# Kernel tuning notes

Measured on AMD Instinct MI355X. Metric: run time of the kernel, lower is better.

The kernel has to match this reference:

```python
import jax, jax.numpy as jnp
import numpy as np

B, N, C = 4, 2304, 256
H = 8                      # num_heads
D = C // H                 # head_dim = 32
SCALE = D ** -0.5
H_DS, W_DS = 48, 48
UP = 2                     # spatial_down_ratio
EPS = 1e-5


def setup_inputs() -> dict:
    key = jax.random.key(0)
    ks = jax.random.split(key, 16)
    g = lambda k, shape, s: (jax.random.normal(k, shape, dtype=jnp.float32) * s)
    return {
        "x1": g(ks[0], (B, N, C), 1.0),
        "x2": g(ks[1], (B, N, C), 1.0),
        # attention projections (torch Linear convention: [out, in], no bias)
        "q1_w": g(ks[2], (C, C), C ** -0.5),
        "kv1_w": g(ks[3], (2 * C, C), C ** -0.5),
        "q2_w": g(ks[4], (C, C), C ** -0.5),
        "kv2_w": g(ks[5], (2 * C, C), C ** -0.5),
        # per-head scalar biases
        "beta12": jnp.full((H,), 0.2, dtype=jnp.float32),
        "beta21": jnp.full((H,), 0.1, dtype=jnp.float32),
        # output projections
        "p1_w": g(ks[6], (C, C), (2.0 / C) ** 0.5),
        "p1_b": g(ks[7], (C,), 1e-2),
        "p2_w": g(ks[8], (C, C), (2.0 / C) ** 0.5),
        "p2_b": g(ks[9], (C,), 1e-2),
        # LayerNorm affine params
        "g1": jnp.ones((C,), dtype=jnp.float32),
        "b1": jnp.zeros((C,), dtype=jnp.float32),
        "g2": jnp.ones((C,), dtype=jnp.float32),
        "b2": jnp.zeros((C,), dtype=jnp.float32),
    }


def _heads(x):
    # [B,N,C] -> [B,H,N,D]
    return x.reshape(B, N, H, D).transpose(0, 2, 1, 3)


def _merge(x):
    # [B,H,N,D] -> [B,N,C]
    return x.transpose(0, 2, 1, 3).reshape(B, N, C)


def _cross_attn(q, k, v, beta):
    # scores: [B,H,N,N] with per-head scalar bias
    s = jnp.einsum("bhqd,bhkd->bhqk", q, k) * SCALE + beta[None, :, None, None]
    a = jax.nn.softmax(s, axis=-1)
    return jnp.einsum("bhqk,bhkd->bhqd", a, v)


def _layernorm(x, g, b):
    mu = jnp.mean(x, axis=-1, keepdims=True)
    var = jnp.var(x, axis=-1, keepdims=True)
    return (x - mu) * jax.lax.rsqrt(var + EPS) * g + b


def _forward(x1, x2, q1_w, kv1_w, q2_w, kv2_w, beta12, beta21,
             p1_w, p1_b, p2_w, p2_b, g1, b1, g2, b2):
    q1 = _heads(x1 @ q1_w.T)
    kv1 = x1 @ kv1_w.T          # [B,N,2C]
    k1, v1 = _heads(kv1[..., :C]), _heads(kv1[..., C:])
    q2 = _heads(x2 @ q2_w.T)
    kv2 = x2 @ kv2_w.T
    k2, v2 = _heads(kv2[..., :C]), _heads(kv2[..., C:])

    o1 = _merge(_cross_attn(q1, k2, v2, beta12))   # x1 attends to x2
    o2 = _merge(_cross_attn(q2, k1, v1, beta21))   # x2 attends to x1

    y1 = _layernorm(jax.nn.relu(o1 @ p1_w.T + p1_b), g1, b1)
    y2 = _layernorm(jax.nn.relu(o2 @ p2_w.T + p2_b), g2, b2)

    # [B,N,C] -> [B,C,H_ds,W_ds]
    y1 = y1.transpose(0, 2, 1).reshape(B, C, H_DS, W_DS)
    y2 = y2.transpose(0, 2, 1).reshape(B, C, H_DS, W_DS)

    # bilinear upsample x2, align_corners=False (half-pixel == jax.image default)
    out_shape = (B, C, H_DS * UP, W_DS * UP)
    y1 = jax.image.resize(y1, out_shape, method="bilinear")
    y2 = jax.image.resize(y2, out_shape, method="bilinear")
    return y1, y2


def reference(x1, x2, q1_w, kv1_w, q2_w, kv2_w, beta12, beta21,
              p1_w, p1_b, p2_w, p2_b, g1, b1, g2, b2):
    return _forward(x1, x2, q1_w, kv1_w, q2_w, kv2_w, beta12, beta21,
                    p1_w, p1_b, p2_w, p2_b, g1, b1, g2, b2)
```

## Files before the change

kernel.cpp:

```cpp
#include <hip/hip_runtime.h>
#include <math.h>


typedef __attribute__((ext_vector_type(8))) short short8;
typedef __attribute__((ext_vector_type(4))) float f32x4;
typedef __attribute__((ext_vector_type(16))) float f32x16;
typedef __attribute__((ext_vector_type(2))) unsigned uint32x2;

#define MFMA16(a, b, c) __builtin_amdgcn_mfma_f32_16x16x32_bf16((a), (b), (c), 0, 0, 0)
#define MFMA32(a, b, c) __builtin_amdgcn_mfma_f32_32x32x16_bf16((a), (b), (c), 0, 0, 0)

__device__ __forceinline__ float bf2f(ushort u) {
    union { unsigned u; float f; } x; x.u = ((unsigned)u) << 16; return x.f;
}
__device__ __forceinline__ ushort f2bf(float f) {
    union { float f; unsigned u; } x; x.f = f;
    unsigned u = x.u;
    return (ushort)((u + 0x7fffu + ((u >> 16) & 1u)) >> 16);
}
__device__ __forceinline__ unsigned cvt_pk_bf16(float a, float b) {
    unsigned r;
    asm("v_cvt_pk_bf16_f32 %0, %1, %2" : "=v"(r) : "v"(a), "v"(b));
    return r;
}
__device__ __forceinline__ float fast_ex2(float x) {
    float r;
    asm("v_exp_f32 %0, %1" : "=v"(r) : "v"(x));
    return r;
}
__device__ __forceinline__ void plswap(unsigned &a, unsigned &b) {
    uint32x2 r = __builtin_amdgcn_permlane32_swap(a, b, false, false);
    a = r[0]; b = r[1];
}

__global__ void sniff_kernel(const ushort* __restrict__ x, int* __restrict__ flag)
{
    int lane = threadIdx.x;
    ushort u = x[lane * 2];
    int e = (u >> 7) & 0xFF;
    int outlier = (e < 100 || e > 135) ? 1 : 0;
    unsigned long long m = __ballot(outlier);
    if (lane == 0) *flag = (__popcll(m) >= 16) ? 1 : 0;
}

__global__ __launch_bounds__(256) void convert_params(
    const void* s0, const void* s1, const void* s2, const void* s3,
    const void* s4, const void* s5, const void* s6, const void* s7,
    const void* s8, const void* s9, const void* s10, const void* s11,
    ushort* __restrict__ dst, const int* __restrict__ flag)
{
    int idx = blockIdx.x * 256 + threadIdx.x;
    if (idx >= 525824) return;
    const void* src; int off;
    if      (idx < 65536)  { src = s0;  off = idx; }
    else if (idx < 196608) { src = s1;  off = idx - 65536; }
    else if (idx < 262144) { src = s2;  off = idx - 196608; }
    else if (idx < 393216) { src = s3;  off = idx - 262144; }
    else if (idx < 458752) { src = s4;  off = idx - 393216; }
    else if (idx < 524288) { src = s5;  off = idx - 458752; }
    else if (idx < 524544) { src = s6;  off = idx - 524288; }
    else if (idx < 524800) { src = s7;  off = idx - 524544; }
    else if (idx < 525056) { src = s8;  off = idx - 524800; }
    else if (idx < 525312) { src = s9;  off = idx - 525056; }
    else if (idx < 525568) { src = s10; off = idx - 525312; }
    else                   { src = s11; off = idx - 525568; }
    ushort v = (*flag) ? f2bf(((const float*)src)[off])
                       : ((const ushort*)src)[off];
    dst[idx] = v;
}

__global__ __launch_bounds__(256) void convert_x(
    const void* __restrict__ x1, const void* __restrict__ x2,
    ushort* __restrict__ o1, ushort* __restrict__ o2,
    const int* __restrict__ flag)
{
    int idx = blockIdx.x * 256 + threadIdx.x;
    int which = idx >= 294912;
    int off = (which ? idx - 294912 : idx) * 8;
    const void* src = which ? x2 : x1;
    ushort* dst = which ? o2 : o1;
    if (*flag) {
        const float* p = (const float*)src + off;
        float4 a = *(const float4*)p;
        float4 c = *(const float4*)(p + 4);
        uint4 u;
        u.x = cvt_pk_bf16(a.x, a.y);
        u.y = cvt_pk_bf16(a.z, a.w);
        u.z = cvt_pk_bf16(c.x, c.y);
        u.w = cvt_pk_bf16(c.z, c.w);
        *(uint4*)(dst + off) = u;
    } else {
        *(uint4*)(dst + off) = *(const uint4*)((const ushort*)src + off);
    }
}

__global__ __launch_bounds__(256) void gemm_bt(
    const void* __restrict__ Ain, const ushort* __restrict__ W,
    ushort* __restrict__ C, const ushort* __restrict__ bias,
    int M, int N, int K, int relu, const int* __restrict__ dflag, int a_ext,
    int mode, ushort* __restrict__ Kh, ushort* __restrict__ Vt,
    const ushort* __restrict__ W2, const ushort* __restrict__ bias2,
    ushort* __restrict__ Kh2, ushort* __restrict__ Vt2, int mhalf)
{
    __shared__ __align__(16) ushort As[64][40];
    __shared__ __align__(16) ushort Ws[64][40];

    const int m0 = blockIdx.x * 64;
    const int n0 = blockIdx.y * 64;
    const int tid = threadIdx.x;
    const int w = tid >> 6;
    const int lane = tid & 63;
    const int lm = lane & 15;
    const int quad = lane >> 4;
    const int a32 = a_ext ? *dflag : 0;

    const int side = (mhalf && m0 >= mhalf) ? 1 : 0;
    const ushort* Wu = side ? W2 : W;
    const ushort* bu = side ? bias2 : bias;
    ushort* Khu = side ? Kh2 : Kh;
    ushort* Vtu = side ? Vt2 : Vt;

    const f32x4 Z4 = {0.f, 0.f, 0.f, 0.f};
    f32x4 acc[4];
    for (int j = 0; j < 4; j++) acc[j] = Z4;

    const ushort* A16 = (const ushort*)Ain;
    const float*  A32 = (const float*)Ain;
    const int row = tid >> 2, off = (tid & 3) * 8;

    for (int k0 = 0; k0 < K; k0 += 32) {
        __syncthreads();
        if (a32) {
            const float* p0 = A32 + (size_t)(m0 + row) * K + k0 + off;
            float4 f0 = *(const float4*)p0;
            float4 f1 = *(const float4*)(p0 + 4);
            uint4 t0;
            t0.x = cvt_pk_bf16(f0.x, f0.y);
            t0.y = cvt_pk_bf16(f0.z, f0.w);
            t0.z = cvt_pk_bf16(f1.x, f1.y);
            t0.w = cvt_pk_bf16(f1.z, f1.w);
            *(uint4*)&As[row][off] = t0;
        } else {
            *(uint4*)&As[row][off] =
                *(const uint4*)(A16 + (size_t)(m0 + row) * K + k0 + off);
        }
        *(uint4*)&Ws[row][off] =
            *(const uint4*)(Wu + (size_t)(n0 + row) * K + k0 + off);
        __syncthreads();

        short8 af = *(const short8*)&As[w * 16 + lm][quad * 8];
        for (int nt = 0; nt < 4; nt++) {
            short8 wf = *(const short8*)&Ws[nt * 16 + lm][quad * 8];
            acc[nt] = MFMA16(af, wf, acc[nt]);
        }
    }

    const int grow = m0 + w * 16 + quad * 4;
    const int grel = grow - (side ? mhalf : 0);
    if (mode == 1) {
        const float QSC = 0.17677669529663687f * 1.4426950408889634f;
        int bb = grel / 2304;
        int tok = grel - bb * 2304;
        for (int nt = 0; nt < 4; nt++) {
            int col = n0 + nt * 16 + lm;
            if (col < 256) {
                for (int r = 0; r < 4; r++)
                    C[(size_t)(grow + r) * 256 + col] = f2bf(acc[nt][r] * QSC);
            } else if (col < 512) {
                int c2 = col - 256, hh = c2 >> 5, d = c2 & 31;
                for (int r = 0; r < 4; r++)
                    Khu[(((size_t)bb * 8 + hh) * 2304 + tok + r) * 32 + d] = f2bf(acc[nt][r]);
            } else {
                int c2 = col - 512, hh = c2 >> 5, d = c2 & 31;
                uint2 o;
                o.x = cvt_pk_bf16(acc[nt][0], acc[nt][1]);
                o.y = cvt_pk_bf16(acc[nt][2], acc[nt][3]);
                *(uint2*)&Vtu[(((size_t)bb * 8 + hh) * 32 + d) * 2304 + tok] = o;
            }
        }
    } else {
        for (int nt = 0; nt < 4; nt++) {
            int col = n0 + nt * 16 + lm;
            float bv = bu ? bf2f(bu[col]) : 0.f;
            for (int r = 0; r < 4; r++) {
                float v = acc[nt][r] + bv;
                if (relu) v = fmaxf(v, 0.f);
                C[(size_t)(grow + r) * N + col] = f2bf(v);
            }
        }
    }
}

__global__ __launch_bounds__(128) void attn_kernel(
    const ushort* __restrict__ Qa, const ushort* __restrict__ Kha,
    const ushort* __restrict__ Vta, ushort* __restrict__ Oa,
    const ushort* __restrict__ Qb, const ushort* __restrict__ Khb2,
    const ushort* __restrict__ Vtb2, ushort* __restrict__ Ob)
{
    const int sid = blockIdx.x;
    const int qb = blockIdx.y;
    const int side = sid >> 5;
    const int bh = sid & 31;
    const ushort* Q  = side ? Qb   : Qa;
    const ushort* Kh = side ? Khb2 : Kha;
    const ushort* Vt = side ? Vtb2 : Vta;
    ushort* O        = side ? Ob   : Oa;

    const int b = bh >> 3, h = bh & 7;
    const int tid = threadIdx.x;
    const int w = tid >> 6, lane = tid & 63;
    const int l31 = lane & 31, hl = lane >> 5;

    const int qrow = qb * 64 + w * 32 + l31;
    const ushort* qp = Q + ((size_t)b * 2304 + qrow) * 256 + h * 32 + hl * 8;
    const short8 qf0 = *(const short8*)qp;
    const short8 qf1 = *(const short8*)(qp + 16);

    f32x16 o0, o1;
    #pragma unroll
    for (int i = 0; i < 16; i++) { o0[i] = 0.f; o1[i] = 0.f; }
    const f32x16 Z16 = o0;
    float l = 0.f;

    const ushort* kp0 = Kh + (size_t)bh * 2304 * 32 + (size_t)l31 * 32 + hl * 8;
    const ushort* vp0 = Vt + (size_t)bh * 32 * 2304 + (size_t)l31 * 2304 + hl * 8;

#define LOADT(kf0v, kf1v, vf0v, vf1v, t) { \
    const ushort* _kp = kp0 + (size_t)(t) * 1024; \
    kf0v = *(const short8*)_kp; \
    kf1v = *(const short8*)(_kp + 16); \
    const ushort* _vp = vp0 + (t) * 32; \
    vf0v = *(const short8*)_vp; \
    vf1v = *(const short8*)(_vp + 16); \
}
#define COMP(kf0v, kf1v, vf0v, vf1v, oacc) { \
    f32x16 s = MFMA32(kf0v, qf0, Z16); \
    s = MFMA32(kf1v, qf1, s); \
    float p[16]; \
    _Pragma("unroll") \
    for (int i = 0; i < 16; i++) p[i] = fast_ex2(s[i]); \
    l += (((p[0] + p[1]) + (p[2] + p[3])) + ((p[4] + p[5]) + (p[6] + p[7]))) \
       + (((p[8] + p[9]) + (p[10] + p[11])) + ((p[12] + p[13]) + (p[14] + p[15]))); \
    unsigned c0 = cvt_pk_bf16(p[0],  p[1]); \
    unsigned c1 = cvt_pk_bf16(p[2],  p[3]); \
    unsigned c2 = cvt_pk_bf16(p[4],  p[5]); \
    unsigned c3 = cvt_pk_bf16(p[6],  p[7]); \
    unsigned c4 = cvt_pk_bf16(p[8],  p[9]); \
    unsigned c5 = cvt_pk_bf16(p[10], p[11]); \
    unsigned c6 = cvt_pk_bf16(p[12], p[13]); \
    unsigned c7 = cvt_pk_bf16(p[14], p[15]); \
    plswap(c0, c2); plswap(c1, c3); plswap(c4, c6); plswap(c5, c7); \
    union { unsigned u[4]; short8 s8; } pA, pB; \
    pA.u[0] = c0; pA.u[1] = c1; pA.u[2] = c2; pA.u[3] = c3; \
    pB.u[0] = c4; pB.u[1] = c5; pB.u[2] = c6; pB.u[3] = c7; \
    oacc = MFMA32(vf0v, pA.s8, oacc); \
    oacc = MFMA32(vf1v, pB.s8, oacc); \
}

    short8 ka0, ka1, va0, va1;
    short8 kb0, kb1, vb0, vb1;

    LOADT(ka0, ka1, va0, va1, 0);
    LOADT(kb0, kb1, vb0, vb1, 1);

    for (int t = 0; t < 72; t += 2) {
        COMP(ka0, ka1, va0, va1, o0);
        { int ta = t + 2 < 72 ? t + 2 : 70; LOADT(ka0, ka1, va0, va1, ta); }
        COMP(kb0, kb1, vb0, vb1, o1);
        { int tb = t + 3 < 72 ? t + 3 : 71; LOADT(kb0, kb1, vb0, vb1, tb); }
    }
#undef LOADT
#undef COMP

    l += __shfl_xor(l, 32, 64);
    float rl = 1.f / l;
    ushort* op = O + ((size_t)b * 2304 + qrow) * 256 + h * 32 + hl * 4;
    #pragma unroll
    for (int g = 0; g < 4; g++) {
        float e0 = (o0[4 * g]     + o1[4 * g])     * rl;
        float e1 = (o0[4 * g + 1] + o1[4 * g + 1]) * rl;
        float e2 = (o0[4 * g + 2] + o1[4 * g + 2]) * rl;
        float e3 = (o0[4 * g + 3] + o1[4 * g + 3]) * rl;
        uint2 o;
        o.x = cvt_pk_bf16(e0, e1);
        o.y = cvt_pk_bf16(e2, e3);
        *(uint2*)(op + 8 * g) = o;
    }
}

__global__ __launch_bounds__(256) void lnt_kernel(
    const ushort* __restrict__ Z, const ushort* __restrict__ G1,
    const ushort* __restrict__ B1, const ushort* __restrict__ G2,
    const ushort* __restrict__ B2, ushort* __restrict__ Yt)
{
    __shared__ ushort T[256][72];

    const int tid = threadIdx.x;
    const int tok0 = blockIdx.x * 32;
    const int half = (tok0 >= 9216) ? 1 : 0;
    const int tr = tok0 - half * 9216;
    const int bb = tr / 2304;
    const int tokb = tr - bb * 2304;

    const int tok_l = tid >> 3;
    const int cq = tid & 7;

    const ushort* zp = Z + ((size_t)(tok0 + tok_l)) * 256 + cq * 32;
    uint dd[16];
    for (int i = 0; i < 4; i++) {
        uint4 v = *(const uint4*)(zp + i * 8);
        dd[i * 4 + 0] = v.x; dd[i * 4 + 1] = v.y;
        dd[i * 4 + 2] = v.z; dd[i * 4 + 3] = v.w;
    }
    float s = 0.f, q = 0.f;
    for (int e = 0; e < 16; e++) {
        float x0 = bf2f((ushort)dd[e]);
        float x1 = bf2f((ushort)(dd[e] >> 16));
        s += x0 + x1;
        q += x0 * x0 + x1 * x1;
    }
    s += __shfl_xor(s, 1, 64); q += __shfl_xor(q, 1, 64);
    s += __shfl_xor(s, 2, 64); q += __shfl_xor(q, 2, 64);
    s += __shfl_xor(s, 4, 64); q += __shfl_xor(q, 4, 64);
    float mu = s * (1.f / 256.f);
    float var = q * (1.f / 256.f) - mu * mu;
    float rs = rsqrtf(var + 1e-5f);

    const ushort* Gs = half ? G2 : G1;
    const ushort* Bs = half ? B2 : B1;
    const int col = tok_l + 4 * cq;

    for (int i = 0; i < 4; i++) {
        int cb = cq * 32 + i * 8;
        uint4 gv = *(const uint4*)(Gs + cb);
        uint4 bv = *(const uint4*)(Bs + cb);
        uint gg[4] = {gv.x, gv.y, gv.z, gv.w};
        uint bw[4] = {bv.x, bv.y, bv.z, bv.w};
        for (int k = 0; k < 4; k++) {
            uint u = dd[i * 4 + k];
            float x0 = bf2f((ushort)u), x1 = bf2f((ushort)(u >> 16));
            float y0 = (x0 - mu) * rs * bf2f((ushort)gg[k]) + bf2f((ushort)bw[k]);
            float y1 = (x1 - mu) * rs * bf2f((ushort)(gg[k] >> 16))
                     + bf2f((ushort)(bw[k] >> 16));
            int c = cb + 2 * k;
            T[c][col]     = f2bf(y0);
            T[c + 1][col] = f2bf(y1);
        }
    }
    __syncthreads();

    const int c_row = tid >> 3;
    const int tq = (tid & 7) * 4;
    const size_t obase = ((size_t)((half * 4 + bb) * 256)) * 2304 + tokb + tq;
    for (int i = 0; i < 8; i++) {
        int c = c_row + 32 * i;
        uint2 v = *(const uint2*)&T[c][tq + 4 * i];
        *(uint2*)(Yt + obase + (size_t)c * 2304) = v;
    }
}

__global__ __launch_bounds__(256) void upsample_kernel(
    const ushort* __restrict__ Yt, float* __restrict__ out)
{
    int idx = blockIdx.x * 256 + threadIdx.x;
    int m  = idx % 48;
    int t  = idx / 48;
    int oi = t % 96;
    int bc = t / 96;

    float fi = oi * 0.5f - 0.25f;
    int i0 = (int)floorf(fi);
    float wi = fi - (float)i0;
    int i1 = i0 + 1 < 47 ? i0 + 1 : 47;
    i0 = i0 > 0 ? i0 : 0;
    int jm = m - 1 > 0 ? m - 1 : 0;
    int jp = m + 1 < 47 ? m + 1 : 47;

    const ushort* r0 = Yt + (size_t)bc * 2304 + i0 * 48;
    const ushort* r1 = Yt + (size_t)bc * 2304 + i1 * 48;
    float a0 = bf2f(r0[jm]), b0 = bf2f(r0[m]), c0 = bf2f(r0[jp]);
    float a1 = bf2f(r1[jm]), b1 = bf2f(r1[m]), c1 = bf2f(r1[jp]);
    float u = 1.f - wi;
    float ha = u * a0 + wi * a1;
    float hb = u * b0 + wi * b1;
    float hc = u * c0 + wi * c1;
    float2 o;
    o.x = 0.25f * ha + 0.75f * hb;
    o.y = 0.75f * hb + 0.25f * hc;
    *(float2*)(out + (size_t)bc * 9216 + oi * 96 + m * 2) = o;
}

extern "C" void kernel_launch(void* const* d_in, const int* in_sizes, int n_in,
                              void* d_out, int out_size, void* d_ws, size_t ws_size,
                              hipStream_t stream)
{
    (void)in_sizes; (void)n_in; (void)out_size; (void)ws_size;

    ushort* ws  = (ushort*)d_ws;
    ushort* Q1  = ws;
    ushort* Q2  = Q1  + 2359296;
    ushort* KV1 = Q2  + 2359296;
    ushort* KV2 = KV1 + 4718592;
    ushort* wc  = KV2 + 4718592;
    int*    dflag = (int*)(wc + 525824);

    ushort* cqkv1w = wc;
    ushort* cqkv2w = wc + 196608;
    ushort* cp1w  = wc + 393216;
    ushort* cp2w  = wc + 458752;
    ushort* cp1b  = wc + 524288;
    ushort* cp2b  = wc + 524544;
    ushort* cg1   = wc + 524800;
    ushort* cb1   = wc + 525056;
    ushort* cg2   = wc + 525312;
    ushort* cb2   = wc + 525568;

    float*  outf = (float*)d_out;
    ushort* O1  = (ushort*)d_out;
    ushort* O2  = O1 + 2359296;
    ushort* Xb1 = O2 + 2359296;
    ushort* Xb2 = Xb1 + 2359296;
    ushort* Z1  = KV2;
    ushort* Yt  = Q1;
    (void)Q2; (void)O2; (void)Xb2;

    dim3 blk(256);
    sniff_kernel<<<dim3(1), dim3(64), 0, stream>>>((const ushort*)d_in[0], dflag);
    convert_params<<<dim3(2054), blk, 0, stream>>>(
        d_in[2], d_in[3], d_in[4], d_in[5], d_in[8], d_in[10],
        d_in[9], d_in[11], d_in[12], d_in[13], d_in[14], d_in[15],
        wc, dflag);
    convert_x<<<dim3(2304), blk, 0, stream>>>(d_in[0], d_in[1], Xb1, Xb2, dflag);

    gemm_bt<<<dim3(288, 12), blk, 0, stream>>>(Xb1, cqkv1w, Q1, nullptr,
        18432, 768, 256, 0, dflag, 0, 1, KV1, KV1 + 2359296,
        cqkv2w, nullptr, KV2, KV2 + 2359296, 9216);

    attn_kernel<<<dim3(64, 36), dim3(128), 0, stream>>>(
        Q1, KV2, KV2 + 2359296, O1,
        Q2, KV1, KV1 + 2359296, O2);

    gemm_bt<<<dim3(288, 4), blk, 0, stream>>>(O1, cp1w, Z1, cp1b,
        18432, 256, 256, 1, dflag, 0, 0, nullptr, nullptr,
        cp2w, cp2b, nullptr, nullptr, 9216);

    lnt_kernel<<<dim3(576), blk, 0, stream>>>(Z1, cg1, cb1, cg2, cb2, Yt);

    upsample_kernel<<<dim3(36864), blk, 0, stream>>>(Yt, outf);
}
```

Before: 303.9 us.

## Process two query tiles per wave and tile K/V layout for contiguous loads

The QKV GEMM epilogue now writes K and V^T into 32-token / 16-token tiled blocks so each attention wave's K and V fragment loads come from contiguous 1KB chunks instead of strided rows. The attention kernel now gives each wave 64 query rows (two 32-row sets) that share every loaded K/V tile, which halves K/V global traffic per query and halves the grid. In exchange each wave holds more registers (two Q fragment sets, two accumulators), the grid has fewer blocks, and the two key-parity accumulators of the old loop are gone, leaving a single dependent accumulator chain per query set.

```diff
diff --git a/kernel.cpp b/kernel.cpp
--- a/kernel.cpp
+++ b/kernel.cpp
@@ -168,14 +168,18 @@
                     C[(size_t)(grow + r) * 256 + col] = f2bf(acc[nt][r] * QSC);
             } else if (col < 512) {
                 int c2 = col - 256, hh = c2 >> 5, d = c2 & 31;
+                size_t kb = ((size_t)(bb * 8 + hh) * 72 + (tok >> 5)) * 1024
+                          + (size_t)(d >> 4) * 512 + (size_t)(d & 15);
                 for (int r = 0; r < 4; r++)
-                    Khu[(((size_t)bb * 8 + hh) * 2304 + tok + r) * 32 + d] = f2bf(acc[nt][r]);
+                    Khu[kb + (size_t)((tok + r) & 31) * 16] = f2bf(acc[nt][r]);
             } else {
                 int c2 = col - 512, hh = c2 >> 5, d = c2 & 31;
+                size_t vb = ((size_t)(bb * 8 + hh) * 144 + (tok >> 4)) * 512
+                          + (size_t)d * 16 + (size_t)(tok & 15);
                 uint2 o;
                 o.x = cvt_pk_bf16(acc[nt][0], acc[nt][1]);
                 o.y = cvt_pk_bf16(acc[nt][2], acc[nt][3]);
-                *(uint2*)&Vtu[(((size_t)bb * 8 + hh) * 32 + d) * 2304 + tok] = o;
+                *(uint2*)&Vtu[vb] = o;
             }
         }
     } else {
@@ -211,36 +215,40 @@
     const int w = tid >> 6, lane = tid & 63;
     const int l31 = lane & 31, hl = lane >> 5;
 
-    const int qrow = qb * 64 + w * 32 + l31;
-    const ushort* qp = Q + ((size_t)b * 2304 + qrow) * 256 + h * 32 + hl * 8;
-    const short8 qf0 = *(const short8*)qp;
-    const short8 qf1 = *(const short8*)(qp + 16);
-
-    f32x16 o0, o1;
+    const int qrow0 = qb * 128 + w * 64 + l31;
+    const int qrow1 = qrow0 + 32;
+    const ushort* qp0 = Q + ((size_t)b * 2304 + qrow0) * 256 + h * 32 + hl * 8;
+    const ushort* qp1 = Q + ((size_t)b * 2304 + qrow1) * 256 + h * 32 + hl * 8;
+    const short8 qf0a = *(const short8*)qp0;
+    const short8 qf1a = *(const short8*)(qp0 + 16);
+    const short8 qf0b = *(const short8*)qp1;
+    const short8 qf1b = *(const short8*)(qp1 + 16);
+
+    f32x16 oa, ob;
     #pragma unroll
-    for (int i = 0; i < 16; i++) { o0[i] = 0.f; o1[i] = 0.f; }
-    const f32x16 Z16 = o0;
-    float l = 0.f;
-
-    const ushort* kp0 = Kh + (size_t)bh * 2304 * 32 + (size_t)l31 * 32 + hl * 8;
-    const ushort* vp0 = Vt + (size_t)bh * 32 * 2304 + (size_t)l31 * 2304 + hl * 8;
+    for (int i = 0; i < 16; i++) { oa[i] = 0.f; ob[i] = 0.f; }
+    const f32x16 Z16 = oa;
+    float la = 0.f, lb = 0.f;
+
+    const ushort* kp0 = Kh + (size_t)bh * 73728 + l31 * 16 + hl * 8;
+    const ushort* vp0 = Vt + (size_t)bh * 73728 + l31 * 16 + hl * 8;
 
 #define LOADT(kf0v, kf1v, vf0v, vf1v, t) { \
     const ushort* _kp = kp0 + (size_t)(t) * 1024; \
     kf0v = *(const short8*)_kp; \
-    kf1v = *(const short8*)(_kp + 16); \
-    const ushort* _vp = vp0 + (t) * 32; \
+    kf1v = *(const short8*)(_kp + 512); \
+    const ushort* _vp = vp0 + (size_t)(t) * 1024; \
     vf0v = *(const short8*)_vp; \
-    vf1v = *(const short8*)(_vp + 16); \
-}
-#define COMP(kf0v, kf1v, vf0v, vf1v, oacc) { \
-    f32x16 s = MFMA32(kf0v, qf0, Z16); \
-    s = MFMA32(kf1v, qf1, s); \
+    vf1v = *(const short8*)(_vp + 512); \
+}
+#define QSET(kf0v, kf1v, vf0v, vf1v, qf0v, qf1v, oacc, lacc) { \
+    f32x16 s = MFMA32(kf0v, qf0v, Z16); \
+    s = MFMA32(kf1v, qf1v, s); \
     float p[16]; \
     _Pragma("unroll") \
     for (int i = 0; i < 16; i++) p[i] = fast_ex2(s[i]); \
-    l += (((p[0] + p[1]) + (p[2] + p[3])) + ((p[4] + p[5]) + (p[6] + p[7]))) \
-       + (((p[8] + p[9]) + (p[10] + p[11])) + ((p[12] + p[13]) + (p[14] + p[15]))); \
+    lacc += (((p[0] + p[1]) + (p[2] + p[3])) + ((p[4] + p[5]) + (p[6] + p[7]))) \
+          + (((p[8] + p[9]) + (p[10] + p[11])) + ((p[12] + p[13]) + (p[14] + p[15]))); \
     unsigned c0 = cvt_pk_bf16(p[0],  p[1]); \
     unsigned c1 = cvt_pk_bf16(p[2],  p[3]); \
     unsigned c2 = cvt_pk_bf16(p[4],  p[5]); \
@@ -256,35 +264,42 @@
     oacc = MFMA32(vf0v, pA.s8, oacc); \
     oacc = MFMA32(vf1v, pB.s8, oacc); \
 }
-
-    short8 ka0, ka1, va0, va1;
-    short8 kb0, kb1, vb0, vb1;
-
-    LOADT(ka0, ka1, va0, va1, 0);
-    LOADT(kb0, kb1, vb0, vb1, 1);
+#define COMP(kf0v, kf1v, vf0v, vf1v) { \
+    QSET(kf0v, kf1v, vf0v, vf1v, qf0a, qf1a, oa, la); \
+    QSET(kf0v, kf1v, vf0v, vf1v, qf0b, qf1b, ob, lb); \
+}
+
+    short8 kA0, kA1, vA0, vA1;
+    short8 kB0, kB1, vB0, vB1;
+
+    LOADT(kA0, kA1, vA0, vA1, 0);
+    LOADT(kB0, kB1, vB0, vB1, 1);
 
     for (int t = 0; t < 72; t += 2) {
-        COMP(ka0, ka1, va0, va1, o0);
-        { int ta = t + 2 < 72 ? t + 2 : 70; LOADT(ka0, ka1, va0, va1, ta); }
-        COMP(kb0, kb1, vb0, vb1, o1);
-        { int tb = t + 3 < 72 ? t + 3 : 71; LOADT(kb0, kb1, vb0, vb1, tb); }
+        COMP(kA0, kA1, vA0, vA1);
+        { int ta = t + 2 < 72 ? t + 2 : 70; LOADT(kA0, kA1, vA0, vA1, ta); }
+        COMP(kB0, kB1, vB0, vB1);
+        { int tb = t + 3 < 72 ? t + 3 : 71; LOADT(kB0, kB1, vB0, vB1, tb); }
     }
 #undef LOADT
+#undef QSET
 #undef COMP
 
-    l += __shfl_xor(l, 32, 64);
-    float rl = 1.f / l;
-    ushort* op = O + ((size_t)b * 2304 + qrow) * 256 + h * 32 + hl * 4;
+    la += __shfl_xor(la, 32, 64);
+    lb += __shfl_xor(lb, 32, 64);
+    float ra = 1.f / la, rb = 1.f / lb;
+    ushort* op0 = O + ((size_t)b * 2304 + qrow0) * 256 + h * 32 + hl * 4;
+    ushort* op1 = O + ((size_t)b * 2304 + qrow1) * 256 + h * 32 + hl * 4;
     #pragma unroll
     for (int g = 0; g < 4; g++) {
-        float e0 = (o0[4 * g]     + o1[4 * g])     * rl;
-        float e1 = (o0[4 * g + 1] + o1[4 * g + 1]) * rl;
-        float e2 = (o0[4 * g + 2] + o1[4 * g + 2]) * rl;
-        float e3 = (o0[4 * g + 3] + o1[4 * g + 3]) * rl;
         uint2 o;
-        o.x = cvt_pk_bf16(e0, e1);
-        o.y = cvt_pk_bf16(e2, e3);
-        *(uint2*)(op + 8 * g) = o;
+        o.x = cvt_pk_bf16(oa[4 * g] * ra, oa[4 * g + 1] * ra);
+        o.y = cvt_pk_bf16(oa[4 * g + 2] * ra, oa[4 * g + 3] * ra);
+        *(uint2*)(op0 + 8 * g) = o;
+        uint2 o2;
+        o2.x = cvt_pk_bf16(ob[4 * g] * rb, ob[4 * g + 1] * rb);
+        o2.y = cvt_pk_bf16(ob[4 * g + 2] * rb, ob[4 * g + 3] * rb);
+        *(uint2*)(op1 + 8 * g) = o2;
     }
 }
 
@@ -436,7 +451,7 @@
         18432, 768, 256, 0, dflag, 0, 1, KV1, KV1 + 2359296,
         cqkv2w, nullptr, KV2, KV2 + 2359296, 9216);
 
-    attn_kernel<<<dim3(64, 36), dim3(128), 0, stream>>>(
+    attn_kernel<<<dim3(64, 18), dim3(128), 0, stream>>>(
         Q1, KV2, KV2 + 2359296, O1,
         Q2, KV1, KV1 + 2359296, O2);
 
```

After: 284.3 us. 1.07x faster.
